# Kernel optimization log

Measured on AMD Instinct MI355X. Metric: run time of the kernel, lower is better.

The kernel has to match this reference:

```python
import jax, jax.numpy as jnp
import numpy as np

EPS = 1e-5

def layernorm(t, gamma, beta):
    mu = jnp.mean(t, axis=-1, keepdims=True)
    var = jnp.mean(jnp.square(t - mu), axis=-1, keepdims=True)
    return (t - mu) * jax.lax.rsqrt(var + EPS) * gamma + beta

def setup_inputs() -> dict:
    key = jax.random.key(0)
    ks = jax.random.split(key, 9)
    B, M, N, C, D = 4, 4096, 32, 256, 128
    x = jax.random.normal(ks[0], (B, M, C), dtype=jnp.float32)
    y = jax.random.normal(ks[1], (B, M, N, C), dtype=jnp.float32)
    z = jax.random.normal(ks[2], (B, M, N, 1), dtype=jnp.float32)
    s = 1.0 / np.sqrt(C)
    Wq = jax.random.normal(ks[3], (C, D), dtype=jnp.float32) * s
    bq = jnp.zeros((D,), dtype=jnp.float32)
    Wk = jax.random.normal(ks[4], (C, D), dtype=jnp.float32) * s
    bk = jnp.zeros((D,), dtype=jnp.float32)
    q_gamma = jnp.ones((C,), dtype=jnp.float32)
    q_beta = jnp.zeros((C,), dtype=jnp.float32)
    k_gamma = jnp.ones((C,), dtype=jnp.float32)
    k_beta = jnp.zeros((C,), dtype=jnp.float32)
    return {"x": x, "y": y, "z": z, "q_gamma": q_gamma, "q_beta": q_beta,
            "Wq": Wq, "bq": bq, "k_gamma": k_gamma, "k_beta": k_beta,
            "Wk": Wk, "bk": bk}

def reference(x, y, z, q_gamma, q_beta, Wq, bq, k_gamma, k_beta, Wk, bk):
    D = Wq.shape[1]
    scale = D ** (-0.5)
    q = layernorm(x, q_gamma, q_beta) @ Wq + bq          # (B, M, D)
    k = layernorm(y, k_gamma, k_beta) @ Wk + bk          # (B, M, N, D)
    # single query vs N keys per node: (B, M, N)
    dot = scale * jnp.einsum('bmd,bmnd->bmn', q, k)
    attn = jax.nn.softmax(dot, axis=-1)[..., None]       # (B, M, N, 1)
    a = jnp.sum(attn * z, axis=-2)                       # (B, M, 1)
    return a
```

## Files before the change

kernel.cpp:

```cpp
#include <hip/hip_runtime.h>
#include <math.h>

#define NROWS 16384
#define NN 32
#define NC 256
#define ND 128
#define RB 8
#define LNEPS 1e-5f
#define SCALE 0.08838834764831845f

typedef float vfloat4 __attribute__((ext_vector_type(4)));

#define OFF_MT   0
#define OFF_UVEC 65536
#define OFF_VV   65792
#define OFF_M1   66048
#define OFF_WG   66304
#define OFF_SCAL 66560

__global__ __launch_bounds__(256)
void ca_prep_a(const float* __restrict__ Wq, const float* __restrict__ Wk,
               const float* __restrict__ qg, const float* __restrict__ qb,
               const float* __restrict__ kg, float* __restrict__ ws) {
    __shared__ __align__(16) float wkrow[ND];
    __shared__ float red[8];
    const int j = blockIdx.x;
    const int c = threadIdx.x;
    const int lane = c & 63, wv = c >> 6;
    if (c < ND / 4) *(float4*)(wkrow + 4 * c) = *(const float4*)(Wk + j * ND + 4 * c);
    __syncthreads();
    float m = 0.f;
    #pragma unroll 8
    for (int d = 0; d < ND; d += 4) {
        const float4 wq4 = *(const float4*)(Wq + c * ND + d);
        const float4 wk4 = *(const float4*)(wkrow + d);
        m += wq4.x * wk4.x + wq4.y * wk4.y + wq4.z * wk4.z + wq4.w * wk4.w;
    }
    const float kgj = kg[j];
    const float mpp = kgj * qg[c] * m;
    ws[OFF_MT + c * NC + j] = mpp;
    float a = mpp, b = kgj * m * qb[c];
    #pragma unroll
    for (int s = 1; s < 64; s <<= 1) { a += __shfl_xor(a, s, 64); b += __shfl_xor(b, s, 64); }
    if (lane == 0) { red[wv] = a; red[4 + wv] = b; }
    __syncthreads();
    if (c == 0) {
        ws[OFF_UVEC + j] = red[0] + red[1] + red[2] + red[3];
        ws[OFF_VV + j]   = red[4] + red[5] + red[6] + red[7];
    }
}

__global__ __launch_bounds__(256)
void ca_prep_b(const float* __restrict__ Wq, const float* __restrict__ Wk,
               const float* __restrict__ qg, const float* __restrict__ qb,
               const float* __restrict__ kg, const float* __restrict__ kb,
               const float* __restrict__ bq, const float* __restrict__ bk,
               float* __restrict__ ws) {
    __shared__ float h[ND];
    __shared__ float htmp[2][ND];
    __shared__ float red[16];
    const int t = threadIdx.x, lane = t & 63, wv = t >> 6;
    {
        float s = 0.f;
        const float* mrow = ws + OFF_MT + t * NC;
        #pragma unroll 8
        for (int j2 = 0; j2 < NC; j2 += 4) {
            const float4 m4 = *(const float4*)(mrow + j2);
            s += (m4.x + m4.y) + (m4.z + m4.w);
        }
        ws[OFF_M1 + t] = s;
    }
    {
        const int d = t & (ND - 1), half = t >> 7;
        float s = 0.f;
        #pragma unroll 8
        for (int j = half * 128; j < half * 128 + 128; ++j) s += Wk[j * ND + d] * kb[j];
        htmp[half][d] = s;
    }
    __syncthreads();
    if (t < ND) h[t] = bk[t] + htmp[0][t] + htmp[1][t];
    __syncthreads();
    float vvj;
    {
        float s = 0.f;
        #pragma unroll 8
        for (int d = 0; d < ND; d += 4) {
            const float4 w4 = *(const float4*)(Wk + t * ND + d);
            const float4 b4 = *(const float4*)(bq + d);
            s += w4.x * b4.x + w4.y * b4.y + w4.z * b4.z + w4.w * b4.w;
        }
        vvj = ws[OFF_VV + t] + kg[t] * s;
        ws[OFF_VV + t] = vvj;
    }
    float w = 0.f;
    #pragma unroll 8
    for (int d = 0; d < ND; d += 4) {
        const float4 w4 = *(const float4*)(Wq + t * ND + d);
        w += w4.x * h[d] + w4.y * h[d + 1] + w4.z * h[d + 2] + w4.w * h[d + 3];
    }
    ws[OFF_WG + t] = qg[t] * w;
    float r0 = qg[t] * w;
    float r1 = qb[t] * w + ((t < ND) ? bq[t] * h[t] : 0.f);
    float r2 = ws[OFF_UVEC + t];
    float r3 = vvj;
    #pragma unroll
    for (int s = 1; s < 64; s <<= 1) {
        r0 += __shfl_xor(r0, s, 64); r1 += __shfl_xor(r1, s, 64);
        r2 += __shfl_xor(r2, s, 64); r3 += __shfl_xor(r3, s, 64);
    }
    if (lane == 0) { red[wv] = r0; red[4 + wv] = r1; red[8 + wv] = r2; red[12 + wv] = r3; }
    __syncthreads();
    if (t == 0) {
        ws[OFF_SCAL + 0] = red[0] + red[1] + red[2] + red[3];
        ws[OFF_SCAL + 1] = red[4] + red[5] + red[6] + red[7];
        ws[OFF_SCAL + 2] = red[8] + red[9] + red[10] + red[11];
        ws[OFF_SCAL + 3] = red[12] + red[13] + red[14] + red[15];
    }
}

__global__ __launch_bounds__(256, 4)
void ca_main(const float* __restrict__ x, const float* __restrict__ y,
             const float* __restrict__ z, const float* __restrict__ ws,
             float* __restrict__ out) {
    __shared__ __align__(16) float xs[RB * NC];
    __shared__ __align__(16) float tp[4 * RB * NC];
    const int tid = threadIdx.x;
    const int lane = tid & 63;
    const int wv = tid >> 6;
    const int row0 = blockIdx.x * RB;

    float mu_[2], rstd_[2], cst_[2], sgr_[2];

    {
        const float4 wg4 = *(const float4*)(ws + OFF_WG + 4 * lane);
        const float4 m14 = *(const float4*)(ws + OFF_M1 + 4 * lane);
        const float s0 = ws[OFF_SCAL + 0], s1c = ws[OFF_SCAL + 1];
        const float s2c = ws[OFF_SCAL + 2], s3c = ws[OFF_SCAL + 3];
        #pragma unroll
        for (int jj = 0; jj < 2; ++jj) {
            const int r = 2 * wv + jj;
            const float4 x4 = *(const float4*)(x + (size_t)(row0 + r) * NC + 4 * lane);
            *(float4*)(xs + r * NC + 4 * lane) = x4;
            float a = (x4.x + x4.y) + (x4.z + x4.w);
            float b = x4.x * x4.x + x4.y * x4.y + x4.z * x4.z + x4.w * x4.w;
            float cw = x4.x * wg4.x + x4.y * wg4.y + x4.z * wg4.z + x4.w * wg4.w;
            float dm = x4.x * m14.x + x4.y * m14.y + x4.z * m14.z + x4.w * m14.w;
            #pragma unroll
            for (int s = 1; s < 64; s <<= 1) {
                a += __shfl_xor(a, s, 64); b += __shfl_xor(b, s, 64);
                cw += __shfl_xor(cw, s, 64); dm += __shfl_xor(dm, s, 64);
            }
            const float mu = a * (1.f / NC);
            const float var = b * (1.f / NC) - mu * mu;
            const float rstd = rsqrtf(var + LNEPS);
            mu_[jj] = mu; rstd_[jj] = rstd;
            cst_[jj] = rstd * (cw - mu * s0) + s1c;
            sgr_[jj] = rstd * (dm - mu * s2c) + s3c;
        }
    }
    __syncthreads();

    {
        float acc[RB][4];
        #pragma unroll
        for (int r = 0; r < RB; ++r) { acc[r][0] = acc[r][1] = acc[r][2] = acc[r][3] = 0.f; }
        const float* Mt = ws + OFF_MT;
        const int cb = 64 * wv;
        #pragma unroll 2
        for (int cc = 0; cc < 64; cc += 4) {
            const int c = cb + cc;
            const float4 m0  = *(const float4*)(Mt + (c + 0) * NC + 4 * lane);
            const float4 m1v = *(const float4*)(Mt + (c + 1) * NC + 4 * lane);
            const float4 m2  = *(const float4*)(Mt + (c + 2) * NC + 4 * lane);
            const float4 m3  = *(const float4*)(Mt + (c + 3) * NC + 4 * lane);
            #pragma unroll
            for (int r = 0; r < RB; ++r) {
                const float4 xv = *(const float4*)(xs + r * NC + c);
                acc[r][0] = fmaf(xv.x, m0.x, fmaf(xv.y, m1v.x, fmaf(xv.z, m2.x, fmaf(xv.w, m3.x, acc[r][0]))));
                acc[r][1] = fmaf(xv.x, m0.y, fmaf(xv.y, m1v.y, fmaf(xv.z, m2.y, fmaf(xv.w, m3.y, acc[r][1]))));
                acc[r][2] = fmaf(xv.x, m0.z, fmaf(xv.y, m1v.z, fmaf(xv.z, m2.z, fmaf(xv.w, m3.z, acc[r][2]))));
                acc[r][3] = fmaf(xv.x, m0.w, fmaf(xv.y, m1v.w, fmaf(xv.z, m2.w, fmaf(xv.w, m3.w, acc[r][3]))));
            }
        }
        #pragma unroll
        for (int r = 0; r < RB; ++r) {
            float4 o; o.x = acc[r][0]; o.y = acc[r][1]; o.z = acc[r][2]; o.w = acc[r][3];
            *(float4*)(tp + (wv * RB + r) * NC + 4 * lane) = o;
        }
    }
    __syncthreads();

    {
        const float4 u4 = *(const float4*)(ws + OFF_UVEC + 4 * lane);
        const float4 v4 = *(const float4*)(ws + OFF_VV + 4 * lane);
        #pragma unroll
        for (int jj = 0; jj < 2; ++jj) {
            const int r = 2 * wv + jj;
            const float4 t0 = *(const float4*)(tp + (0 * RB + r) * NC + 4 * lane);
            const float4 t1 = *(const float4*)(tp + (1 * RB + r) * NC + 4 * lane);
            const float4 t2 = *(const float4*)(tp + (2 * RB + r) * NC + 4 * lane);
            const float4 t3 = *(const float4*)(tp + (3 * RB + r) * NC + 4 * lane);
            const float rstd = rstd_[jj], mu = mu_[jj];
            float4 gp;
            gp.x = rstd * ((t0.x + t1.x + t2.x + t3.x) - mu * u4.x) + v4.x;
            gp.y = rstd * ((t0.y + t1.y + t2.y + t3.y) - mu * u4.y) + v4.y;
            gp.z = rstd * ((t0.z + t1.z + t2.z + t3.z) - mu * u4.z) + v4.z;
            gp.w = rstd * ((t0.w + t1.w + t2.w + t3.w) - mu * u4.w) + v4.w;
            *(float4*)(tp + r * NC + 4 * lane) = gp;
        }
    }

    {
        const int g = lane >> 4;
        const int i = lane & 15;
        const int sig = 8 * g + (lane & 7);
        #pragma unroll 1
        for (int jj = 0; jj < 2; ++jj) {
            const int r = 2 * wv + jj;
            const size_t row = (size_t)row0 + r;
            const float* gl = tp + r * NC + 4 * i;
            const vfloat4 g0 = *(const vfloat4*)(gl + 0);
            const vfloat4 g1 = *(const vfloat4*)(gl + 64);
            const vfloat4 g2 = *(const vfloat4*)(gl + 128);
            const vfloat4 g3 = *(const vfloat4*)(gl + 192);
            const float cst = cst_[jj], sg = sgr_[jj];
            const float* kb0 = y + row * (size_t)(NN * NC) + (8 * g) * NC + 4 * i;
            const float zv = z[row * NN + sig];
            float dv = 0.f;
            vfloat4 ya0, yb0, yc0, yd0, ya1, yb1, yc1, yd1;
            vfloat4 ya2, yb2, yc2, yd2, ya3, yb3, yc3, yd3;

#define LOADS(S, K) \
            ya##S = *(const vfloat4*)(kb0 + (K) * NC + 0); \
            yb##S = *(const vfloat4*)(kb0 + (K) * NC + 64); \
            yc##S = *(const vfloat4*)(kb0 + (K) * NC + 128); \
            yd##S = *(const vfloat4*)(kb0 + (K) * NC + 192);

#define REDK(S, K) { \
            float s1 = (((ya##S.x + ya##S.y) + (ya##S.z + ya##S.w)) + ((yb##S.x + yb##S.y) + (yb##S.z + yb##S.w))) \
                     + (((yc##S.x + yc##S.y) + (yc##S.z + yc##S.w)) + ((yd##S.x + yd##S.y) + (yd##S.z + yd##S.w))); \
            float s2 = ya##S.x*ya##S.x + ya##S.y*ya##S.y + ya##S.z*ya##S.z + ya##S.w*ya##S.w \
                     + yb##S.x*yb##S.x + yb##S.y*yb##S.y + yb##S.z*yb##S.z + yb##S.w*yb##S.w \
                     + yc##S.x*yc##S.x + yc##S.y*yc##S.y + yc##S.z*yc##S.z + yc##S.w*yc##S.w \
                     + yd##S.x*yd##S.x + yd##S.y*yd##S.y + yd##S.z*yd##S.z + yd##S.w*yd##S.w; \
            float s3 = ya##S.x*g0.x + ya##S.y*g0.y + ya##S.z*g0.z + ya##S.w*g0.w \
                     + yb##S.x*g1.x + yb##S.y*g1.y + yb##S.z*g1.z + yb##S.w*g1.w \
                     + yc##S.x*g2.x + yc##S.y*g2.y + yc##S.z*g2.z + yc##S.w*g2.w \
                     + yd##S.x*g3.x + yd##S.y*g3.y + yd##S.z*g3.z + yd##S.w*g3.w; \
            _Pragma("unroll") \
            for (int s = 1; s < 16; s <<= 1) { \
                s1 += __shfl_xor(s1, s, 64); \
                s2 += __shfl_xor(s2, s, 64); \
                s3 += __shfl_xor(s3, s, 64); \
            } \
            const float mun = s1 * (1.f / NC); \
            const float varn = s2 * (1.f / NC) - mun * mun; \
            const float rsd = rsqrtf(varn + LNEPS); \
            const float dt = SCALE * (rsd * (s3 - mun * sg) + cst); \
            dv = ((lane & 7) == (K)) ? dt : dv; }

            LOADS(0, 0) LOADS(1, 1) LOADS(2, 2) LOADS(3, 3)
            REDK(0, 0) LOADS(0, 4)
            REDK(1, 1) LOADS(1, 5)
            REDK(2, 2) LOADS(2, 6)
            REDK(3, 3) LOADS(3, 7)
            REDK(0, 4) REDK(1, 5) REDK(2, 6) REDK(3, 7)
#undef LOADS
#undef REDK

            float mx = dv;
            mx = fmaxf(mx, __shfl_xor(mx, 1, 64));
            mx = fmaxf(mx, __shfl_xor(mx, 2, 64));
            mx = fmaxf(mx, __shfl_xor(mx, 4, 64));
            mx = fmaxf(mx, __shfl_xor(mx, 16, 64));
            mx = fmaxf(mx, __shfl_xor(mx, 32, 64));
            const float e = __expf(dv - mx);
            float num = e * zv, den = e;
            num += __shfl_xor(num, 1, 64);  den += __shfl_xor(den, 1, 64);
            num += __shfl_xor(num, 2, 64);  den += __shfl_xor(den, 2, 64);
            num += __shfl_xor(num, 4, 64);  den += __shfl_xor(den, 4, 64);
            num += __shfl_xor(num, 16, 64); den += __shfl_xor(den, 16, 64);
            num += __shfl_xor(num, 32, 64); den += __shfl_xor(den, 32, 64);
            if (lane == 0) out[row] = num / den;
        }
    }
}

extern "C" void kernel_launch(void* const* d_in, const int* in_sizes, int n_in,
                              void* d_out, int out_size, void* d_ws, size_t ws_size,
                              hipStream_t stream) {
    const float* x  = (const float*)d_in[0];
    const float* y  = (const float*)d_in[1];
    const float* z  = (const float*)d_in[2];
    const float* qg = (const float*)d_in[3];
    const float* qb = (const float*)d_in[4];
    const float* Wq = (const float*)d_in[5];
    const float* bq = (const float*)d_in[6];
    const float* kg = (const float*)d_in[7];
    const float* kb = (const float*)d_in[8];
    const float* Wk = (const float*)d_in[9];
    const float* bk = (const float*)d_in[10];
    float* out = (float*)d_out;
    float* ws = (float*)d_ws;

    ca_prep_a<<<NC, 256, 0, stream>>>(Wq, Wk, qg, qb, kg, ws);
    ca_prep_b<<<1, 256, 0, stream>>>(Wq, Wk, qg, qb, kg, kb, bq, bk, ws);
    ca_main<<<NROWS / RB, 256, 0, stream>>>(x, y, z, ws, out);
}
```

Before: 150.4 us.

## Compute per-wave projection for own rows, drop shared partial-sum buffer and barriers

Each wave now computes the full 256-wide projection for its own two rows instead of a 64-channel slice for all eight rows. This removes the 32KB shared partial-sum buffer and the two block barriers, and the projected vector is handed to the key loop through lane shuffles rather than LDS reads. The cost is that every wave streams the whole Mt matrix, roughly quadrupling Mt cache traffic per block. In exchange, shared-memory use drops sharply, which should allow more resident blocks to hide y-load latency.

```diff
diff --git a/kernel.cpp b/kernel.cpp
--- a/kernel.cpp
+++ b/kernel.cpp
@@ -123,13 +123,13 @@
              const float* __restrict__ z, const float* __restrict__ ws,
              float* __restrict__ out) {
     __shared__ __align__(16) float xs[RB * NC];
-    __shared__ __align__(16) float tp[4 * RB * NC];
     const int tid = threadIdx.x;
     const int lane = tid & 63;
     const int wv = tid >> 6;
     const int row0 = blockIdx.x * RB;
-
-    float mu_[2], rstd_[2], cst_[2], sgr_[2];
+    const int rA = 2 * wv, rB = 2 * wv + 1;
+
+    float muA, muB, rstdA, rstdB, cstA, cstB, sgA, sgB;
 
     {
         const float4 wg4 = *(const float4*)(ws + OFF_WG + 4 * lane);
@@ -153,61 +153,45 @@
             const float mu = a * (1.f / NC);
             const float var = b * (1.f / NC) - mu * mu;
             const float rstd = rsqrtf(var + LNEPS);
-            mu_[jj] = mu; rstd_[jj] = rstd;
-            cst_[jj] = rstd * (cw - mu * s0) + s1c;
-            sgr_[jj] = rstd * (dm - mu * s2c) + s3c;
-        }
-    }
-    __syncthreads();
-
-    {
-        float acc[RB][4];
-        #pragma unroll
-        for (int r = 0; r < RB; ++r) { acc[r][0] = acc[r][1] = acc[r][2] = acc[r][3] = 0.f; }
+            if (jj == 0) { muA = mu; rstdA = rstd; cstA = rstd * (cw - mu * s0) + s1c; sgA = rstd * (dm - mu * s2c) + s3c; }
+            else         { muB = mu; rstdB = rstd; cstB = rstd * (cw - mu * s0) + s1c; sgB = rstd * (dm - mu * s2c) + s3c; }
+        }
+    }
+
+    vfloat4 gpA, gpB;
+    {
+        float a0 = 0.f, a1 = 0.f, a2 = 0.f, a3 = 0.f;
+        float b0 = 0.f, b1 = 0.f, b2 = 0.f, b3 = 0.f;
         const float* Mt = ws + OFF_MT;
-        const int cb = 64 * wv;
-        #pragma unroll 2
-        for (int cc = 0; cc < 64; cc += 4) {
-            const int c = cb + cc;
-            const float4 m0  = *(const float4*)(Mt + (c + 0) * NC + 4 * lane);
-            const float4 m1v = *(const float4*)(Mt + (c + 1) * NC + 4 * lane);
-            const float4 m2  = *(const float4*)(Mt + (c + 2) * NC + 4 * lane);
-            const float4 m3  = *(const float4*)(Mt + (c + 3) * NC + 4 * lane);
-            #pragma unroll
-            for (int r = 0; r < RB; ++r) {
-                const float4 xv = *(const float4*)(xs + r * NC + c);
-                acc[r][0] = fmaf(xv.x, m0.x, fmaf(xv.y, m1v.x, fmaf(xv.z, m2.x, fmaf(xv.w, m3.x, acc[r][0]))));
-                acc[r][1] = fmaf(xv.x, m0.y, fmaf(xv.y, m1v.y, fmaf(xv.z, m2.y, fmaf(xv.w, m3.y, acc[r][1]))));
-                acc[r][2] = fmaf(xv.x, m0.z, fmaf(xv.y, m1v.z, fmaf(xv.z, m2.z, fmaf(xv.w, m3.z, acc[r][2]))));
-                acc[r][3] = fmaf(xv.x, m0.w, fmaf(xv.y, m1v.w, fmaf(xv.z, m2.w, fmaf(xv.w, m3.w, acc[r][3]))));
-            }
-        }
-        #pragma unroll
-        for (int r = 0; r < RB; ++r) {
-            float4 o; o.x = acc[r][0]; o.y = acc[r][1]; o.z = acc[r][2]; o.w = acc[r][3];
-            *(float4*)(tp + (wv * RB + r) * NC + 4 * lane) = o;
-        }
-    }
-    __syncthreads();
-
-    {
-        const float4 u4 = *(const float4*)(ws + OFF_UVEC + 4 * lane);
-        const float4 v4 = *(const float4*)(ws + OFF_VV + 4 * lane);
-        #pragma unroll
-        for (int jj = 0; jj < 2; ++jj) {
-            const int r = 2 * wv + jj;
-            const float4 t0 = *(const float4*)(tp + (0 * RB + r) * NC + 4 * lane);
-            const float4 t1 = *(const float4*)(tp + (1 * RB + r) * NC + 4 * lane);
-            const float4 t2 = *(const float4*)(tp + (2 * RB + r) * NC + 4 * lane);
-            const float4 t3 = *(const float4*)(tp + (3 * RB + r) * NC + 4 * lane);
-            const float rstd = rstd_[jj], mu = mu_[jj];
-            float4 gp;
-            gp.x = rstd * ((t0.x + t1.x + t2.x + t3.x) - mu * u4.x) + v4.x;
-            gp.y = rstd * ((t0.y + t1.y + t2.y + t3.y) - mu * u4.y) + v4.y;
-            gp.z = rstd * ((t0.z + t1.z + t2.z + t3.z) - mu * u4.z) + v4.z;
-            gp.w = rstd * ((t0.w + t1.w + t2.w + t3.w) - mu * u4.w) + v4.w;
-            *(float4*)(tp + r * NC + 4 * lane) = gp;
-        }
+        const float* xsa = xs + rA * NC;
+        const float* xsb = xs + rB * NC;
+        #pragma unroll 4
+        for (int c = 0; c < NC; c += 4) {
+            const vfloat4 m0  = *(const vfloat4*)(Mt + (c + 0) * NC + 4 * lane);
+            const vfloat4 m1v = *(const vfloat4*)(Mt + (c + 1) * NC + 4 * lane);
+            const vfloat4 m2  = *(const vfloat4*)(Mt + (c + 2) * NC + 4 * lane);
+            const vfloat4 m3  = *(const vfloat4*)(Mt + (c + 3) * NC + 4 * lane);
+            const vfloat4 xa = *(const vfloat4*)(xsa + c);
+            const vfloat4 xb = *(const vfloat4*)(xsb + c);
+            a0 = fmaf(xa.x, m0.x, fmaf(xa.y, m1v.x, fmaf(xa.z, m2.x, fmaf(xa.w, m3.x, a0))));
+            a1 = fmaf(xa.x, m0.y, fmaf(xa.y, m1v.y, fmaf(xa.z, m2.y, fmaf(xa.w, m3.y, a1))));
+            a2 = fmaf(xa.x, m0.z, fmaf(xa.y, m1v.z, fmaf(xa.z, m2.z, fmaf(xa.w, m3.z, a2))));
+            a3 = fmaf(xa.x, m0.w, fmaf(xa.y, m1v.w, fmaf(xa.z, m2.w, fmaf(xa.w, m3.w, a3))));
+            b0 = fmaf(xb.x, m0.x, fmaf(xb.y, m1v.x, fmaf(xb.z, m2.x, fmaf(xb.w, m3.x, b0))));
+            b1 = fmaf(xb.x, m0.y, fmaf(xb.y, m1v.y, fmaf(xb.z, m2.y, fmaf(xb.w, m3.y, b1))));
+            b2 = fmaf(xb.x, m0.z, fmaf(xb.y, m1v.z, fmaf(xb.z, m2.z, fmaf(xb.w, m3.z, b2))));
+            b3 = fmaf(xb.x, m0.w, fmaf(xb.y, m1v.w, fmaf(xb.z, m2.w, fmaf(xb.w, m3.w, b3))));
+        }
+        const vfloat4 u4 = *(const vfloat4*)(ws + OFF_UVEC + 4 * lane);
+        const vfloat4 v4 = *(const vfloat4*)(ws + OFF_VV + 4 * lane);
+        gpA.x = rstdA * (a0 - muA * u4.x) + v4.x;
+        gpA.y = rstdA * (a1 - muA * u4.y) + v4.y;
+        gpA.z = rstdA * (a2 - muA * u4.z) + v4.z;
+        gpA.w = rstdA * (a3 - muA * u4.w) + v4.w;
+        gpB.x = rstdB * (b0 - muB * u4.x) + v4.x;
+        gpB.y = rstdB * (b1 - muB * u4.y) + v4.y;
+        gpB.z = rstdB * (b2 - muB * u4.z) + v4.z;
+        gpB.w = rstdB * (b3 - muB * u4.w) + v4.w;
     }
 
     {
@@ -216,14 +200,19 @@
         const int sig = 8 * g + (lane & 7);
         #pragma unroll 1
         for (int jj = 0; jj < 2; ++jj) {
-            const int r = 2 * wv + jj;
-            const size_t row = (size_t)row0 + r;
-            const float* gl = tp + r * NC + 4 * i;
-            const vfloat4 g0 = *(const vfloat4*)(gl + 0);
-            const vfloat4 g1 = *(const vfloat4*)(gl + 64);
-            const vfloat4 g2 = *(const vfloat4*)(gl + 128);
-            const vfloat4 g3 = *(const vfloat4*)(gl + 192);
-            const float cst = cst_[jj], sg = sgr_[jj];
+            const size_t row = (size_t)row0 + 2 * wv + jj;
+            const float cst = jj ? cstB : cstA;
+            const float sg  = jj ? sgB  : sgA;
+            const vfloat4 gp_r = jj ? gpB : gpA;
+            vfloat4 g0, g1, g2, g3;
+            g0.x = __shfl(gp_r.x, i, 64);      g0.y = __shfl(gp_r.y, i, 64);
+            g0.z = __shfl(gp_r.z, i, 64);      g0.w = __shfl(gp_r.w, i, 64);
+            g1.x = __shfl(gp_r.x, i + 16, 64); g1.y = __shfl(gp_r.y, i + 16, 64);
+            g1.z = __shfl(gp_r.z, i + 16, 64); g1.w = __shfl(gp_r.w, i + 16, 64);
+            g2.x = __shfl(gp_r.x, i + 32, 64); g2.y = __shfl(gp_r.y, i + 32, 64);
+            g2.z = __shfl(gp_r.z, i + 32, 64); g2.w = __shfl(gp_r.w, i + 32, 64);
+            g3.x = __shfl(gp_r.x, i + 48, 64); g3.y = __shfl(gp_r.y, i + 48, 64);
+            g3.z = __shfl(gp_r.z, i + 48, 64); g3.w = __shfl(gp_r.w, i + 48, 64);
             const float* kb0 = y + row * (size_t)(NN * NC) + (8 * g) * NC + 4 * i;
             const float zv = z[row * NN + sig];
             float dv = 0.f;
```

Measured after the change: 192.1 us. 27.7% more time.

## Stream key rows through LDS with async global_load_lds double buffering

Applied to the files above, without the earlier changes.

Replaces the direct register loads of y rows with asynchronous global-to-LDS copies (global_load_lds) into a per-wave double-buffered staging area. Each wave then computes the layernorm and dot reductions from LDS while the next pair of key rows is in flight, with waits controlled by explicit vmcnt. The normalized query vectors move to a separate xs buffer, and both rows' query registers are loaded up front. This aims to raise memory-level parallelism and cut register pressure in the bandwidth-bound key pass. In exchange it adds LDS traffic and fragile hand-placed waitcnt and sched_barrier ordering.

```diff
diff --git a/kernel.cpp b/kernel.cpp
--- a/kernel.cpp
+++ b/kernel.cpp
@@ -17,6 +17,12 @@
 #define OFF_M1   66048
 #define OFF_WG   66304
 #define OFF_SCAL 66560
+
+__device__ __forceinline__ void gload16(const float* g, float* l) {
+    __builtin_amdgcn_global_load_lds(
+        (__attribute__((address_space(1))) void*)(void*)g,
+        (__attribute__((address_space(3))) void*)l, 16, 0, 0);
+}
 
 __global__ __launch_bounds__(256)
 void ca_prep_a(const float* __restrict__ Wq, const float* __restrict__ Wk,
@@ -206,7 +212,7 @@
             gp.y = rstd * ((t0.y + t1.y + t2.y + t3.y) - mu * u4.y) + v4.y;
             gp.z = rstd * ((t0.z + t1.z + t2.z + t3.z) - mu * u4.z) + v4.z;
             gp.w = rstd * ((t0.w + t1.w + t2.w + t3.w) - mu * u4.w) + v4.w;
-            *(float4*)(tp + r * NC + 4 * lane) = gp;
+            *(float4*)(xs + r * NC + 4 * lane) = gp;
         }
     }
 
@@ -214,39 +220,49 @@
         const int g = lane >> 4;
         const int i = lane & 15;
         const int sig = 8 * g + (lane & 7);
-        #pragma unroll 1
-        for (int jj = 0; jj < 2; ++jj) {
-            const int r = 2 * wv + jj;
-            const size_t row = (size_t)row0 + r;
-            const float* gl = tp + r * NC + 4 * i;
-            const vfloat4 g0 = *(const vfloat4*)(gl + 0);
-            const vfloat4 g1 = *(const vfloat4*)(gl + 64);
-            const vfloat4 g2 = *(const vfloat4*)(gl + 128);
-            const vfloat4 g3 = *(const vfloat4*)(gl + 192);
-            const float cst = cst_[jj], sg = sgr_[jj];
-            const float* kb0 = y + row * (size_t)(NN * NC) + (8 * g) * NC + 4 * i;
-            const float zv = z[row * NN + sig];
-            float dv = 0.f;
-            vfloat4 ya0, yb0, yc0, yd0, ya1, yb1, yc1, yd1;
-            vfloat4 ya2, yb2, yc2, yd2, ya3, yb3, yc3, yd3;
-
-#define LOADS(S, K) \
-            ya##S = *(const vfloat4*)(kb0 + (K) * NC + 0); \
-            yb##S = *(const vfloat4*)(kb0 + (K) * NC + 64); \
-            yc##S = *(const vfloat4*)(kb0 + (K) * NC + 128); \
-            yd##S = *(const vfloat4*)(kb0 + (K) * NC + 192);
-
-#define REDK(S, K) { \
-            float s1 = (((ya##S.x + ya##S.y) + (ya##S.z + ya##S.w)) + ((yb##S.x + yb##S.y) + (yb##S.z + yb##S.w))) \
-                     + (((yc##S.x + yc##S.y) + (yc##S.z + yc##S.w)) + ((yd##S.x + yd##S.y) + (yd##S.z + yd##S.w))); \
-            float s2 = ya##S.x*ya##S.x + ya##S.y*ya##S.y + ya##S.z*ya##S.z + ya##S.w*ya##S.w \
-                     + yb##S.x*yb##S.x + yb##S.y*yb##S.y + yb##S.z*yb##S.z + yb##S.w*yb##S.w \
-                     + yc##S.x*yc##S.x + yc##S.y*yc##S.y + yc##S.z*yc##S.z + yc##S.w*yc##S.w \
-                     + yd##S.x*yd##S.x + yd##S.y*yd##S.y + yd##S.z*yd##S.z + yd##S.w*yd##S.w; \
-            float s3 = ya##S.x*g0.x + ya##S.y*g0.y + ya##S.z*g0.z + ya##S.w*g0.w \
-                     + yb##S.x*g1.x + yb##S.y*g1.y + yb##S.z*g1.z + yb##S.w*g1.w \
-                     + yc##S.x*g2.x + yc##S.y*g2.y + yc##S.z*g2.z + yc##S.w*g2.w \
-                     + yd##S.x*g3.x + yd##S.y*g3.y + yd##S.z*g3.z + yd##S.w*g3.w; \
+        float* stage = tp + wv * 2048;
+
+        const float* glA = xs + (2 * wv + 0) * NC + 4 * i;
+        const vfloat4 A0 = *(const vfloat4*)(glA + 0);
+        const vfloat4 A1 = *(const vfloat4*)(glA + 64);
+        const vfloat4 A2 = *(const vfloat4*)(glA + 128);
+        const vfloat4 A3 = *(const vfloat4*)(glA + 192);
+        const float* glB = xs + (2 * wv + 1) * NC + 4 * i;
+        const vfloat4 B0 = *(const vfloat4*)(glB + 0);
+        const vfloat4 B1 = *(const vfloat4*)(glB + 64);
+        const vfloat4 B2 = *(const vfloat4*)(glB + 128);
+        const vfloat4 B3 = *(const vfloat4*)(glB + 192);
+        const float zvA = z[(size_t)(row0 + 2 * wv + 0) * NN + sig];
+        const float zvB = z[(size_t)(row0 + 2 * wv + 1) * NN + sig];
+        asm volatile("s_waitcnt vmcnt(0)" ::: "memory");
+        __syncthreads();
+
+#define STAGE(r, b) { \
+            gload16(yrow + (8 * 0 + (r)) * NC + 4 * lane, stage + (b) * 1024 + 0 * 256); \
+            gload16(yrow + (8 * 1 + (r)) * NC + 4 * lane, stage + (b) * 1024 + 1 * 256); \
+            gload16(yrow + (8 * 2 + (r)) * NC + 4 * lane, stage + (b) * 1024 + 2 * 256); \
+            gload16(yrow + (8 * 3 + (r)) * NC + 4 * lane, stage + (b) * 1024 + 3 * 256); }
+
+#define ROUND(K, b, WN, STG) { \
+            asm volatile("s_waitcnt vmcnt(" WN ")" ::: "memory"); \
+            __builtin_amdgcn_sched_barrier(0); \
+            const float* kp = stage + (b) * 1024 + g * 256 + 4 * i; \
+            const vfloat4 y0 = *(const vfloat4*)(kp + 0); \
+            const vfloat4 y1 = *(const vfloat4*)(kp + 64); \
+            const vfloat4 y2 = *(const vfloat4*)(kp + 128); \
+            const vfloat4 y3 = *(const vfloat4*)(kp + 192); \
+            float s1 = (((y0.x + y0.y) + (y0.z + y0.w)) + ((y1.x + y1.y) + (y1.z + y1.w))) \
+                     + (((y2.x + y2.y) + (y2.z + y2.w)) + ((y3.x + y3.y) + (y3.z + y3.w))); \
+            float s2 = y0.x*y0.x + y0.y*y0.y + y0.z*y0.z + y0.w*y0.w \
+                     + y1.x*y1.x + y1.y*y1.y + y1.z*y1.z + y1.w*y1.w \
+                     + y2.x*y2.x + y2.y*y2.y + y2.z*y2.z + y2.w*y2.w \
+                     + y3.x*y3.x + y3.y*y3.y + y3.z*y3.z + y3.w*y3.w; \
+            float s3 = y0.x*g0.x + y0.y*g0.y + y0.z*g0.z + y0.w*g0.w \
+                     + y1.x*g1.x + y1.y*g1.y + y1.z*g1.z + y1.w*g1.w \
+                     + y2.x*g2.x + y2.y*g2.y + y2.z*g2.z + y2.w*g2.w \
+                     + y3.x*g3.x + y3.y*g3.y + y3.z*g3.z + y3.w*g3.w; \
+            __builtin_amdgcn_sched_barrier(0); \
+            STG; \
             _Pragma("unroll") \
             for (int s = 1; s < 16; s <<= 1) { \
                 s1 += __shfl_xor(s1, s, 64); \
@@ -259,14 +275,29 @@
             const float dt = SCALE * (rsd * (s3 - mun * sg) + cst); \
             dv = ((lane & 7) == (K)) ? dt : dv; }
 
-            LOADS(0, 0) LOADS(1, 1) LOADS(2, 2) LOADS(3, 3)
-            REDK(0, 0) LOADS(0, 4)
-            REDK(1, 1) LOADS(1, 5)
-            REDK(2, 2) LOADS(2, 6)
-            REDK(3, 3) LOADS(3, 7)
-            REDK(0, 4) REDK(1, 5) REDK(2, 6) REDK(3, 7)
-#undef LOADS
-#undef REDK
+        #pragma unroll
+        for (int jj = 0; jj < 2; ++jj) {
+            const size_t row = (size_t)row0 + 2 * wv + jj;
+            const float cst = jj ? cst_[1] : cst_[0];
+            const float sg  = jj ? sgr_[1] : sgr_[0];
+            const vfloat4 g0 = jj ? B0 : A0;
+            const vfloat4 g1 = jj ? B1 : A1;
+            const vfloat4 g2 = jj ? B2 : A2;
+            const vfloat4 g3 = jj ? B3 : A3;
+            const float zv = jj ? zvB : zvA;
+            const float* yrow = y + row * (size_t)(NN * NC);
+            float dv = 0.f;
+
+            STAGE(0, 0)
+            STAGE(1, 1)
+            ROUND(0, 0, "4", STAGE(2, 0))
+            ROUND(1, 1, "4", STAGE(3, 1))
+            ROUND(2, 0, "4", STAGE(4, 0))
+            ROUND(3, 1, "4", STAGE(5, 1))
+            ROUND(4, 0, "4", STAGE(6, 0))
+            ROUND(5, 1, "4", STAGE(7, 1))
+            ROUND(6, 0, "4", ((void)0))
+            ROUND(7, 1, "0", ((void)0))
 
             float mx = dv;
             mx = fmaxf(mx, __shfl_xor(mx, 1, 64));
@@ -282,7 +313,10 @@
             num += __shfl_xor(num, 16, 64); den += __shfl_xor(den, 16, 64);
             num += __shfl_xor(num, 32, 64); den += __shfl_xor(den, 32, 64);
             if (lane == 0) out[row] = num / den;
-        }
+            asm volatile("s_waitcnt vmcnt(0)" ::: "memory");
+        }
+#undef STAGE
+#undef ROUND
     }
 }
 
```

Result: slower. 159.8 us (+6.2%).
